# Kernel tuning notes

Measured on AMD Instinct MI355X. Metric: run time of the kernel, lower is better.

The kernel has to match this reference:

```python
import jax, jax.numpy as jnp
import numpy as np

NUM_HEADS = 16
EMB = 1024
HEAD_DIM = EMB // NUM_HEADS


def setup_inputs() -> dict:
    key = jax.random.key(0)
    ks = jax.random.split(key, 9)
    N, L = 2, 2048
    return {
        "keys": jax.random.normal(ks[0], (N, L, EMB), dtype=jnp.float32),
        "queries": jax.random.normal(ks[1], (N, L, EMB), dtype=jnp.float32),
        "values": jax.random.normal(ks[2], (N, L, EMB), dtype=jnp.float32),
        "mask": jax.random.randint(ks[3], (N, L), 0, 2, dtype=jnp.int32),
        "Wk": jax.random.normal(ks[4], (HEAD_DIM, HEAD_DIM), dtype=jnp.float32) * 0.05,
        "Wq": jax.random.normal(ks[5], (HEAD_DIM, HEAD_DIM), dtype=jnp.float32) * 0.05,
        "Wv": jax.random.normal(ks[6], (HEAD_DIM, HEAD_DIM), dtype=jnp.float32) * 0.05,
        "Wo": jax.random.normal(ks[7], (EMB, EMB), dtype=jnp.float32) * 0.02,
        "bo": jax.random.normal(ks[8], (EMB,), dtype=jnp.float32) * 0.02,
    }


def reference(keys, queries, values, mask, Wk, Wq, Wv, Wo, bo):
    N, Q, E = queries.shape
    H, D = NUM_HEADS, HEAD_DIM
    # reshape to heads: [N, L, H, D]
    k = keys.reshape(N, -1, H, D) @ Wk.T
    q = queries.reshape(N, -1, H, D) @ Wq.T
    # faithful to source bug: values are the v-projection of the projected queries
    v = q @ Wv.T
    # energy: [N, H, Q, K]
    energy = jnp.einsum("nqhd,nkhd->nhqk", q, k)
    m = mask[:, None, None, :]  # [N,1,1,K]
    energy = jnp.where(m == 0, jnp.float32(-1e20), energy)
    p = jax.nn.softmax(energy / jnp.sqrt(jnp.float32(E)), axis=3)
    attn = jnp.einsum("nhqk,nkhd->nqhd", p, v).reshape(N, Q, E)
    return attn @ Wo.T + bo
```

## Files before the change

### kernel.cpp

```cpp
#include <hip/hip_runtime.h>
#include <hip/hip_bf16.h>
#include <cmath>

constexpr int N_ = 2;
constexpr int L_ = 2048;
constexpr int H_ = 16;
constexpr int E_ = 1024;
constexpr int ROWS_ = N_ * L_ * H_;
constexpr float KSCALE = 0.04508422002778010648f;

typedef __attribute__((ext_vector_type(8))) short bf16x8;
typedef __attribute__((ext_vector_type(4))) float f32x4;
typedef unsigned short ushort_t;
#define MFMA16(a, b, c) __builtin_amdgcn_mfma_f32_16x16x32_bf16(a, b, c, 0, 0, 0)

__device__ __forceinline__ unsigned short f2bf(float x) {
    union { float f; unsigned u; } v; v.f = x;
    return (unsigned short)((v.u + 0x7fffu + ((v.u >> 16) & 1u)) >> 16);
}
__device__ __forceinline__ unsigned pack2(float a, float b) {
    __hip_bfloat162 t = __float22bfloat162_rn(make_float2(a, b));
    union { __hip_bfloat162 h; unsigned u; } v; v.h = t;
    return v.u;
}
__device__ __forceinline__ void plswap32(unsigned &a, unsigned &b) {
    asm("v_permlane32_swap_b32 %0, %1" : "+v"(a), "+v"(b));
}
__device__ __forceinline__ void plswap16(unsigned &a, unsigned &b) {
    asm("v_permlane16_swap_b32 %0, %1" : "+v"(a), "+v"(b));
}

__global__ __launch_bounds__(256) void proj_kernel(
    const float* __restrict__ keys, const float* __restrict__ queries,
    const float* __restrict__ Wk, const float* __restrict__ Wq, const float* __restrict__ Wv,
    ushort_t* __restrict__ qo, ushort_t* __restrict__ ko, ushort_t* __restrict__ vto)
{
    constexpr int P = 72;
    __shared__ __align__(16) ushort_t Xq[64 * P];
    __shared__ __align__(16) ushort_t Xk[64 * P];
    __shared__ __align__(16) ushort_t Wqs[64 * P];
    __shared__ __align__(16) ushort_t Wks[64 * P];
    __shared__ __align__(16) ushort_t Wvs[64 * P];
    const int tid = threadIdx.x;
    const int lt = blockIdx.x & 31;
    const int h  = (blockIdx.x >> 5) & 15;
    const int n  = blockIdx.x >> 9;
    const int r0 = tid >> 4, c4 = (tid & 15) * 4;

#pragma unroll
    for (int j = 0; j < 4; ++j) {
        const int r = r0 + 16 * j;
        const size_t xoff = (size_t)(n * L_ + lt * 64 + r) * E_ + h * 64 + c4;
        const float4 xq = *(const float4*)&queries[xoff];
        const float4 xk = *(const float4*)&keys[xoff];
        const float4 wq = *(const float4*)&Wq[r * 64 + c4];
        const float4 wk = *(const float4*)&Wk[r * 64 + c4];
        const float4 wv = *(const float4*)&Wv[r * 64 + c4];
        *(uint2*)&Xq[r * P + c4]  = make_uint2(pack2(xq.x, xq.y), pack2(xq.z, xq.w));
        *(uint2*)&Xk[r * P + c4]  = make_uint2(pack2(xk.x, xk.y), pack2(xk.z, xk.w));
        *(uint2*)&Wqs[r * P + c4] = make_uint2(pack2(wq.x, wq.y), pack2(wq.z, wq.w));
        *(uint2*)&Wks[r * P + c4] = make_uint2(pack2(wk.x, wk.y), pack2(wk.z, wk.w));
        *(uint2*)&Wvs[r * P + c4] = make_uint2(pack2(wv.x, wv.y), pack2(wv.z, wv.w));
    }
    __syncthreads();

    const int wave = tid >> 6, lane = tid & 63;
    const int quad = lane >> 4, l16 = lane & 15;
    const int arow = (wave * 16 + l16) * P;
    const f32x4 zero = (f32x4){0.f, 0.f, 0.f, 0.f};

    bf16x8 a0 = *(const bf16x8*)&Xq[arow + quad * 8];
    bf16x8 a1 = *(const bf16x8*)&Xq[arow + 32 + quad * 8];
    bf16x8 c0 = *(const bf16x8*)&Xk[arow + quad * 8];
    bf16x8 c1 = *(const bf16x8*)&Xk[arow + 32 + quad * 8];
    f32x4 qf[4], kf[4];
#pragma unroll
    for (int nt = 0; nt < 4; ++nt) {
        const int brow = (nt * 16 + l16) * P;
        f32x4 acc = MFMA16(a0, *(const bf16x8*)&Wqs[brow + quad * 8], zero);
        qf[nt] = MFMA16(a1, *(const bf16x8*)&Wqs[brow + 32 + quad * 8], acc);
        acc = MFMA16(c0, *(const bf16x8*)&Wks[brow + quad * 8], zero);
        kf[nt] = MFMA16(c1, *(const bf16x8*)&Wks[brow + 32 + quad * 8], acc);
    }
    __syncthreads();

    const int crow = wave * 16 + quad * 4;
#pragma unroll
    for (int nt = 0; nt < 4; ++nt)
#pragma unroll
        for (int reg = 0; reg < 4; ++reg) {
            Xq[(crow + reg) * P + nt * 16 + l16]  = f2bf(qf[nt][reg]);
            Wqs[(crow + reg) * P + nt * 16 + l16] = f2bf(kf[nt][reg] * KSCALE);
        }
    asm volatile("s_waitcnt lgkmcnt(0)" ::: "memory");

    bf16x8 va0 = *(const bf16x8*)&Xq[arow + quad * 8];
    bf16x8 va1 = *(const bf16x8*)&Xq[arow + 32 + quad * 8];
    f32x4 vf[4];
#pragma unroll
    for (int nt = 0; nt < 4; ++nt) {
        const int brow = (nt * 16 + l16) * P;
        f32x4 acc = MFMA16(va0, *(const bf16x8*)&Wvs[brow + quad * 8], zero);
        vf[nt] = MFMA16(va1, *(const bf16x8*)&Wvs[brow + 32 + quad * 8], acc);
    }
#pragma unroll
    for (int nt = 0; nt < 4; ++nt)
#pragma unroll
        for (int reg = 0; reg < 4; ++reg)
            Xk[(nt * 16 + l16) * P + crow + reg] = f2bf(vf[nt][reg]);
    __syncthreads();

#pragma unroll
    for (int j = 0; j < 4; ++j) {
        const int r = r0 + 16 * j;
        const size_t qkoff = (size_t)(n * L_ + lt * 64 + r) * E_ + h * 64 + c4;
        *(uint2*)&qo[qkoff] = *(const uint2*)&Xq[r * P + c4];
        *(uint2*)&ko[qkoff] = *(const uint2*)&Wqs[r * P + c4];
        const size_t vtoff = ((size_t)(n * H_ + h) * 64 + r) * L_ + lt * 64 + c4;
        *(uint2*)&vto[vtoff] = *(const uint2*)&Xk[r * P + c4];
    }
}

__global__ __launch_bounds__(512, 4) void attn_kernel(
    const ushort_t* __restrict__ q, const ushort_t* __restrict__ k,
    const ushort_t* __restrict__ vt, const float* __restrict__ maskf,
    ushort_t* __restrict__ attn)
{
    constexpr int PK = 72;
    constexpr int PV = 136;
    constexpr int KP_SZ = 128 * PK;
    constexpr int VP_SZ = 64 * PV;
    __shared__ __align__(16) unsigned char SMEM[(2 * KP_SZ + 2 * VP_SZ) * 2 + 512];
    ushort_t* Kp = (ushort_t*)SMEM;
    ushort_t* Vp = (ushort_t*)(SMEM + 2 * KP_SZ * 2);
    float*    Ls = (float*)(SMEM + (2 * KP_SZ + 2 * VP_SZ) * 2);
    float*    Oc = (float*)SMEM;
    float*    Lp = (float*)(SMEM + 2 * KP_SZ * 2);

    const int g = blockIdx.x;
    const int xcd = g & 7, j0 = g >> 3;
    const int nh = xcd * 4 + (j0 & 3);
    const int qt = j0 >> 2;
    const int n = nh >> 4, h = nh & 15;

    const int tid = threadIdx.x;
    const int wave = tid >> 6, lane = tid & 63;
    const int l16 = lane & 15, quad = lane >> 4;
    const int qg = wave & 3, kg = wave >> 2;
    const int r8 = tid >> 3, c8 = (tid & 7) * 8;
    const int vr8 = tid >> 4, vc8 = (tid & 15) * 8;

    const ushort_t* kh = k  + (size_t)n * L_ * E_ + h * 64;
    const ushort_t* vh = vt + (size_t)(n * H_ + h) * 64 * L_;
    const float*    mh = maskf + n * L_;
    const size_t qrow0 = (size_t)n * L_ + qt * 128 + qg * 32;

    bf16x8 qb[2][2];
#pragma unroll
    for (int st = 0; st < 2; ++st)
#pragma unroll
        for (int c = 0; c < 2; ++c)
            qb[st][c] = *(const bf16x8*)&q[(qrow0 + st * 16 + l16) * E_ + h * 64 + c * 32 + quad * 8];

    uint4 kr[2], vr[2];
#pragma unroll
    for (int j = 0; j < 2; ++j) {
        kr[j] = *(const uint4*)&kh[(size_t)(64 * j + r8) * E_ + c8];
        vr[j] = *(const uint4*)&vh[(size_t)(vr8 + 32 * j) * L_ + vc8];
    }
    f32x4 mf[4];
#pragma unroll
    for (int mk = 0; mk < 4; ++mk) mf[mk] = *(const f32x4*)&mh[kg * 64 + mk * 16 + quad * 4];

#pragma unroll
    for (int j = 0; j < 2; ++j) {
        *(uint4*)&Kp[(64 * j + r8) * PK + c8]  = kr[j];
        *(uint4*)&Vp[(vr8 + 32 * j) * PV + vc8] = vr[j];
    }
    __syncthreads();

    float lacc[2] = {0.f, 0.f};
    f32x4 O[2][4];
#pragma unroll
    for (int st = 0; st < 2; ++st)
#pragma unroll
        for (int dt = 0; dt < 4; ++dt) O[st][dt] = (f32x4){0.f, 0.f, 0.f, 0.f};

    for (int s = 0; s < 16; ++s) {
        const int cur = s & 1, nxt = cur ^ 1;
        const int sn = (s < 15) ? s + 1 : 15;

#pragma unroll
        for (int j = 0; j < 2; ++j) {
            kr[j] = *(const uint4*)&kh[(size_t)(128 * sn + 64 * j + r8) * E_ + c8];
            vr[j] = *(const uint4*)&vh[(size_t)(vr8 + 32 * j) * L_ + 128 * sn + vc8];
        }
        f32x4 mfn[4];
#pragma unroll
        for (int mk = 0; mk < 4; ++mk)
            mfn[mk] = *(const f32x4*)&mh[128 * sn + kg * 64 + mk * 16 + quad * 4];

        bf16x8 kA[4][2];
#pragma unroll
        for (int mk = 0; mk < 4; ++mk)
#pragma unroll
            for (int c = 0; c < 2; ++c)
                kA[mk][c] = *(const bf16x8*)&Kp[cur * KP_SZ + (kg * 64 + mk * 16 + l16) * PK + c * 32 + quad * 8];

        f32x4 sA[2][4];
#pragma unroll
        for (int st = 0; st < 2; ++st)
#pragma unroll
            for (int mk = 0; mk < 4; ++mk) {
                f32x4 acc = mf[mk];
                acc = MFMA16(kA[mk][0], qb[st][0], acc);
                sA[st][mk] = MFMA16(kA[mk][1], qb[st][1], acc);
            }

        bf16x8 vB[4][2];
#pragma unroll
        for (int dt = 0; dt < 4; ++dt)
#pragma unroll
            for (int c = 0; c < 2; ++c)
                vB[dt][c] = *(const bf16x8*)&Vp[cur * VP_SZ + (dt * 16 + l16) * PV + kg * 64 + c * 32 + quad * 8];

        bf16x8 pa[2][2];
#pragma unroll
        for (int st = 0; st < 2; ++st) {
            unsigned u[4][2];
#pragma unroll
            for (int mk = 0; mk < 4; ++mk) {
                const float p0 = __builtin_amdgcn_exp2f(sA[st][mk][0]);
                const float p1 = __builtin_amdgcn_exp2f(sA[st][mk][1]);
                const float p2 = __builtin_amdgcn_exp2f(sA[st][mk][2]);
                const float p3 = __builtin_amdgcn_exp2f(sA[st][mk][3]);
                lacc[st] += (p0 + p1) + (p2 + p3);
                u[mk][0] = pack2(p0, p1);
                u[mk][1] = pack2(p2, p3);
            }
#pragma unroll
            for (int c = 0; c < 2; ++c) {
                union { unsigned w[4]; bf16x8 v; } pw;
#pragma unroll
                for (int hh = 0; hh < 2; ++hh) {
                    unsigned a = u[2 * c][hh], b = u[2 * c + 1][hh];
                    plswap32(a, b);
                    plswap16(a, b);
                    pw.w[hh] = a; pw.w[2 + hh] = b;
                }
                pa[st][c] = pw.v;
            }
        }

#pragma unroll
        for (int st = 0; st < 2; ++st)
#pragma unroll
            for (int dt = 0; dt < 4; ++dt) {
                O[st][dt] = MFMA16(pa[st][0], vB[dt][0], O[st][dt]);
                O[st][dt] = MFMA16(pa[st][1], vB[dt][1], O[st][dt]);
            }

#pragma unroll
        for (int j = 0; j < 2; ++j) {
            *(uint4*)&Kp[nxt * KP_SZ + (64 * j + r8) * PK + c8]   = kr[j];
            *(uint4*)&Vp[nxt * VP_SZ + (vr8 + 32 * j) * PV + vc8] = vr[j];
        }
#pragma unroll
        for (int mk = 0; mk < 4; ++mk) mf[mk] = mfn[mk];
        __syncthreads();
    }

    float vsum[2];
#pragma unroll
    for (int st = 0; st < 2; ++st) {
        float v = lacc[st];
        v += __shfl_xor(v, 16);
        v += __shfl_xor(v, 32);
        vsum[st] = v;
    }

    if (kg == 1) {
#pragma unroll
        for (int st = 0; st < 2; ++st) {
            if (quad == 0) Lp[qg * 32 + st * 16 + l16] = vsum[st];
#pragma unroll
            for (int dt = 0; dt < 4; ++dt)
                *(f32x4*)&Oc[(dt * 16 + l16) * 132 + qg * 32 + st * 16 + quad * 4] = O[st][dt];
        }
    }
    __syncthreads();

    if (kg == 0) {
#pragma unroll
        for (int st = 0; st < 2; ++st) {
#pragma unroll
            for (int dt = 0; dt < 4; ++dt) {
                const f32x4 op = *(const f32x4*)&Oc[(dt * 16 + l16) * 132 + qg * 32 + st * 16 + quad * 4];
                O[st][dt] += op;
            }
            const float vtot = vsum[st] + Lp[qg * 32 + st * 16 + l16];
            if (quad == 0) Ls[qg * 32 + st * 16 + l16] = 1.f / vtot;
        }
        asm volatile("s_waitcnt lgkmcnt(0)" ::: "memory");
        f32x4 linv[2];
#pragma unroll
        for (int st = 0; st < 2; ++st)
            linv[st] = *(const f32x4*)&Ls[qg * 32 + st * 16 + quad * 4];

#pragma unroll
        for (int st = 0; st < 2; ++st)
#pragma unroll
            for (int dt = 0; dt < 4; ++dt)
#pragma unroll
                for (int reg = 0; reg < 4; ++reg) {
                    const size_t row = qrow0 + st * 16 + quad * 4 + reg;
                    attn[row * E_ + h * 64 + dt * 16 + l16] = f2bf(O[st][dt][reg] * linv[st][reg]);
                }
    }
}

__global__ __launch_bounds__(256) void conv_misc_kernel(
    const float* __restrict__ Wo, const int* __restrict__ mask,
    ushort_t* __restrict__ Wob, float* __restrict__ maskf)
{
    if (blockIdx.x < 1024) {
        const int i = (blockIdx.x * 256 + threadIdx.x) * 4;
        const float4 w = *(const float4*)&Wo[i];
        *(uint2*)&Wob[i] = make_uint2(pack2(w.x, w.y), pack2(w.z, w.w));
    } else {
        const int j = (blockIdx.x - 1024) * 256 + threadIdx.x;
        if (j < N_ * L_) maskf[j] = mask[j] ? 0.f : -1e9f;
    }
}

__global__ __launch_bounds__(256) void outproj_kernel(
    const ushort_t* __restrict__ attn, const ushort_t* __restrict__ Wob,
    const float* __restrict__ bo, float* __restrict__ out)
{
    constexpr int P = 72;
    __shared__ __align__(16) ushort_t As[128 * P];
    __shared__ __align__(16) ushort_t Bs[64 * P];
    const int tid = threadIdx.x;
    const int bc = (blockIdx.x & 15) * 64;
    const int br = (blockIdx.x >> 4) * 128;
    const int r0 = tid >> 4, c4 = (tid & 15) * 4;
    const int wave = tid >> 6, lane = tid & 63;
    const int quad = lane >> 4, l16 = lane & 15;

    uint2 ar[8], brg[4];
#pragma unroll
    for (int j = 0; j < 8; ++j)
        ar[j] = *(const uint2*)&attn[(size_t)(br + r0 + 16 * j) * E_ + c4];
#pragma unroll
    for (int j = 0; j < 4; ++j)
        brg[j] = *(const uint2*)&Wob[(size_t)(bc + r0 + 16 * j) * E_ + c4];

    f32x4 acc[2][4];
#pragma unroll
    for (int s = 0; s < 2; ++s)
#pragma unroll
        for (int nt = 0; nt < 4; ++nt) acc[s][nt] = (f32x4){0.f, 0.f, 0.f, 0.f};

    for (int kt = 0; kt < 16; ++kt) {
#pragma unroll
        for (int j = 0; j < 8; ++j) *(uint2*)&As[(r0 + 16 * j) * P + c4] = ar[j];
#pragma unroll
        for (int j = 0; j < 4; ++j) *(uint2*)&Bs[(r0 + 16 * j) * P + c4] = brg[j];
        __syncthreads();
        const int knext = ((kt < 15) ? (kt + 1) : kt) * 64;
#pragma unroll
        for (int j = 0; j < 8; ++j)
            ar[j] = *(const uint2*)&attn[(size_t)(br + r0 + 16 * j) * E_ + knext + c4];
#pragma unroll
        for (int j = 0; j < 4; ++j)
            brg[j] = *(const uint2*)&Wob[(size_t)(bc + r0 + 16 * j) * E_ + knext + c4];

        bf16x8 aw[2][2], bw[4][2];
#pragma unroll
        for (int s = 0; s < 2; ++s)
#pragma unroll
            for (int c = 0; c < 2; ++c)
                aw[s][c] = *(const bf16x8*)&As[(wave * 32 + s * 16 + l16) * P + c * 32 + quad * 8];
#pragma unroll
        for (int nt = 0; nt < 4; ++nt)
#pragma unroll
            for (int c = 0; c < 2; ++c)
                bw[nt][c] = *(const bf16x8*)&Bs[(nt * 16 + l16) * P + c * 32 + quad * 8];
#pragma unroll
        for (int s = 0; s < 2; ++s)
#pragma unroll
            for (int nt = 0; nt < 4; ++nt) {
                acc[s][nt] = MFMA16(aw[s][0], bw[nt][0], acc[s][nt]);
                acc[s][nt] = MFMA16(aw[s][1], bw[nt][1], acc[s][nt]);
            }
        __syncthreads();
    }
#pragma unroll
    for (int s = 0; s < 2; ++s)
#pragma unroll
        for (int nt = 0; nt < 4; ++nt) {
            const float bias = bo[bc + nt * 16 + l16];
#pragma unroll
            for (int reg = 0; reg < 4; ++reg)
                out[(size_t)(br + wave * 32 + s * 16 + quad * 4 + reg) * E_ + bc + nt * 16 + l16] =
                    acc[s][nt][reg] + bias;
        }
}

extern "C" void kernel_launch(void* const* d_in, const int* in_sizes, int n_in,
                              void* d_out, int out_size, void* d_ws, size_t ws_size,
                              hipStream_t stream)
{
    const float* keys    = (const float*)d_in[0];
    const float* queries = (const float*)d_in[1];
    const int*   mask    = (const int*)d_in[3];
    const float* Wk      = (const float*)d_in[4];
    const float* Wq      = (const float*)d_in[5];
    const float* Wv      = (const float*)d_in[6];
    const float* Wo      = (const float*)d_in[7];
    const float* bo      = (const float*)d_in[8];
    float* out = (float*)d_out;

    ushort_t* qbf  = (ushort_t*)d_ws;
    ushort_t* kbf  = qbf + (size_t)ROWS_ * 64;
    ushort_t* vtbf = kbf + (size_t)ROWS_ * 64;
    ushort_t* abf  = vtbf + (size_t)ROWS_ * 64;
    ushort_t* wob  = abf + (size_t)ROWS_ * 64;
    float*    mskf = (float*)(wob + (size_t)E_ * E_);

    conv_misc_kernel<<<1024 + (N_ * L_ + 255) / 256, 256, 0, stream>>>(Wo, mask, wob, mskf);
    proj_kernel<<<N_ * H_ * (L_ / 64), 256, 0, stream>>>(keys, queries, Wk, Wq, Wv,
                                                         qbf, kbf, vtbf);
    attn_kernel<<<N_ * H_ * (L_ / 128), 512, 0, stream>>>(qbf, kbf, vtbf, mskf, abf);
    outproj_kernel<<<(N_ * L_ / 128) * (E_ / 64), 256, 0, stream>>>(abf, wob, bo, out);
}
```

Before: 183.4 us.

## Fuse conversion kernel into projection, compute row sums via MFMA, widen loads

Folds the Wo bf16 conversion and mask preprocessing into the projection kernel as extra blocks, removing one kernel launch. In attention, the softmax denominator is now accumulated with an MFMA against a ones vector instead of scalar adds plus cross-lane shuffles, and s_setprio hints are placed around the MFMA sections. The output projection switches from 8-byte to 16-byte global and LDS accesses, and its MFMA loop is also wrapped with setprio. In exchange the attention loop issues extra MFMAs and the projection kernel runs a larger, mixed-work grid.

```diff
diff --git a/kernel.cpp b/kernel.cpp
--- a/kernel.cpp
+++ b/kernel.cpp
@@ -33,7 +33,9 @@
 __global__ __launch_bounds__(256) void proj_kernel(
     const float* __restrict__ keys, const float* __restrict__ queries,
     const float* __restrict__ Wk, const float* __restrict__ Wq, const float* __restrict__ Wv,
-    ushort_t* __restrict__ qo, ushort_t* __restrict__ ko, ushort_t* __restrict__ vto)
+    ushort_t* __restrict__ qo, ushort_t* __restrict__ ko, ushort_t* __restrict__ vto,
+    const float* __restrict__ Wo, const int* __restrict__ mask,
+    ushort_t* __restrict__ Wob, float* __restrict__ maskf)
 {
     constexpr int P = 72;
     __shared__ __align__(16) ushort_t Xq[64 * P];
@@ -42,6 +44,20 @@
     __shared__ __align__(16) ushort_t Wks[64 * P];
     __shared__ __align__(16) ushort_t Wvs[64 * P];
     const int tid = threadIdx.x;
+
+    if (blockIdx.x >= 1024) {
+        const int b = blockIdx.x - 1024;
+        if (b < 1024) {
+            const int i = (b * 256 + tid) * 4;
+            const float4 w = *(const float4*)&Wo[i];
+            *(uint2*)&Wob[i] = make_uint2(pack2(w.x, w.y), pack2(w.z, w.w));
+        } else {
+            const int j = (b - 1024) * 256 + tid;
+            if (j < N_ * L_) maskf[j] = mask[j] ? 0.f : -1e9f;
+        }
+        return;
+    }
+
     const int lt = blockIdx.x & 31;
     const int h  = (blockIdx.x >> 5) & 15;
     const int n  = blockIdx.x >> 9;
@@ -130,10 +146,9 @@
     constexpr int PV = 136;
     constexpr int KP_SZ = 128 * PK;
     constexpr int VP_SZ = 64 * PV;
-    __shared__ __align__(16) unsigned char SMEM[(2 * KP_SZ + 2 * VP_SZ) * 2 + 512];
+    __shared__ __align__(16) unsigned char SMEM[(2 * KP_SZ + 2 * VP_SZ) * 2];
     ushort_t* Kp = (ushort_t*)SMEM;
     ushort_t* Vp = (ushort_t*)(SMEM + 2 * KP_SZ * 2);
-    float*    Ls = (float*)(SMEM + (2 * KP_SZ + 2 * VP_SZ) * 2);
     float*    Oc = (float*)SMEM;
     float*    Lp = (float*)(SMEM + 2 * KP_SZ * 2);
 
@@ -155,6 +170,10 @@
     const float*    mh = maskf + n * L_;
     const size_t qrow0 = (size_t)n * L_ + qt * 128 + qg * 32;
 
+    bf16x8 onesB;
+#pragma unroll
+    for (int i = 0; i < 8; ++i) onesB[i] = (short)0x3F80;
+
     bf16x8 qb[2][2];
 #pragma unroll
     for (int st = 0; st < 2; ++st)
@@ -179,12 +198,13 @@
     }
     __syncthreads();
 
-    float lacc[2] = {0.f, 0.f};
-    f32x4 O[2][4];
-#pragma unroll
-    for (int st = 0; st < 2; ++st)
+    f32x4 O[2][4], lO[2];
+#pragma unroll
+    for (int st = 0; st < 2; ++st) {
+        lO[st] = (f32x4){0.f, 0.f, 0.f, 0.f};
 #pragma unroll
         for (int dt = 0; dt < 4; ++dt) O[st][dt] = (f32x4){0.f, 0.f, 0.f, 0.f};
+    }
 
     for (int s = 0; s < 16; ++s) {
         const int cur = s & 1, nxt = cur ^ 1;
@@ -208,6 +228,7 @@
                 kA[mk][c] = *(const bf16x8*)&Kp[cur * KP_SZ + (kg * 64 + mk * 16 + l16) * PK + c * 32 + quad * 8];
 
         f32x4 sA[2][4];
+        __builtin_amdgcn_s_setprio(1);
 #pragma unroll
         for (int st = 0; st < 2; ++st)
 #pragma unroll
@@ -216,6 +237,7 @@
                 acc = MFMA16(kA[mk][0], qb[st][0], acc);
                 sA[st][mk] = MFMA16(kA[mk][1], qb[st][1], acc);
             }
+        __builtin_amdgcn_s_setprio(0);
 
         bf16x8 vB[4][2];
 #pragma unroll
@@ -234,7 +256,6 @@
                 const float p1 = __builtin_amdgcn_exp2f(sA[st][mk][1]);
                 const float p2 = __builtin_amdgcn_exp2f(sA[st][mk][2]);
                 const float p3 = __builtin_amdgcn_exp2f(sA[st][mk][3]);
-                lacc[st] += (p0 + p1) + (p2 + p3);
                 u[mk][0] = pack2(p0, p1);
                 u[mk][1] = pack2(p2, p3);
             }
@@ -252,13 +273,18 @@
             }
         }
 
-#pragma unroll
-        for (int st = 0; st < 2; ++st)
+        __builtin_amdgcn_s_setprio(1);
+#pragma unroll
+        for (int st = 0; st < 2; ++st) {
 #pragma unroll
             for (int dt = 0; dt < 4; ++dt) {
                 O[st][dt] = MFMA16(pa[st][0], vB[dt][0], O[st][dt]);
                 O[st][dt] = MFMA16(pa[st][1], vB[dt][1], O[st][dt]);
             }
+            lO[st] = MFMA16(pa[st][0], onesB, lO[st]);
+            lO[st] = MFMA16(pa[st][1], onesB, lO[st]);
+        }
+        __builtin_amdgcn_s_setprio(0);
 
 #pragma unroll
         for (int j = 0; j < 2; ++j) {
@@ -270,27 +296,20 @@
         __syncthreads();
     }
 
-    float vsum[2];
-#pragma unroll
-    for (int st = 0; st < 2; ++st) {
-        float v = lacc[st];
-        v += __shfl_xor(v, 16);
-        v += __shfl_xor(v, 32);
-        vsum[st] = v;
-    }
-
     if (kg == 1) {
 #pragma unroll
         for (int st = 0; st < 2; ++st) {
-            if (quad == 0) Lp[qg * 32 + st * 16 + l16] = vsum[st];
 #pragma unroll
             for (int dt = 0; dt < 4; ++dt)
                 *(f32x4*)&Oc[(dt * 16 + l16) * 132 + qg * 32 + st * 16 + quad * 4] = O[st][dt];
+            if (l16 == 0)
+                *(f32x4*)&Lp[qg * 32 + st * 16 + quad * 4] = lO[st];
         }
     }
     __syncthreads();
 
     if (kg == 0) {
+        f32x4 linv[2];
 #pragma unroll
         for (int st = 0; st < 2; ++st) {
 #pragma unroll
@@ -298,14 +317,11 @@
                 const f32x4 op = *(const f32x4*)&Oc[(dt * 16 + l16) * 132 + qg * 32 + st * 16 + quad * 4];
                 O[st][dt] += op;
             }
-            const float vtot = vsum[st] + Lp[qg * 32 + st * 16 + l16];
-            if (quad == 0) Ls[qg * 32 + st * 16 + l16] = 1.f / vtot;
-        }
-        asm volatile("s_waitcnt lgkmcnt(0)" ::: "memory");
-        f32x4 linv[2];
-#pragma unroll
-        for (int st = 0; st < 2; ++st)
-            linv[st] = *(const f32x4*)&Ls[qg * 32 + st * 16 + quad * 4];
+            const f32x4 lpart = *(const f32x4*)&Lp[qg * 32 + st * 16 + quad * 4];
+#pragma unroll
+            for (int reg = 0; reg < 4; ++reg)
+                linv[st][reg] = 1.f / (lO[st][reg] + lpart[reg]);
+        }
 
 #pragma unroll
         for (int st = 0; st < 2; ++st)
@@ -316,20 +332,6 @@
                     const size_t row = qrow0 + st * 16 + quad * 4 + reg;
                     attn[row * E_ + h * 64 + dt * 16 + l16] = f2bf(O[st][dt][reg] * linv[st][reg]);
                 }
-    }
-}
-
-__global__ __launch_bounds__(256) void conv_misc_kernel(
-    const float* __restrict__ Wo, const int* __restrict__ mask,
-    ushort_t* __restrict__ Wob, float* __restrict__ maskf)
-{
-    if (blockIdx.x < 1024) {
-        const int i = (blockIdx.x * 256 + threadIdx.x) * 4;
-        const float4 w = *(const float4*)&Wo[i];
-        *(uint2*)&Wob[i] = make_uint2(pack2(w.x, w.y), pack2(w.z, w.w));
-    } else {
-        const int j = (blockIdx.x - 1024) * 256 + threadIdx.x;
-        if (j < N_ * L_) maskf[j] = mask[j] ? 0.f : -1e9f;
     }
 }
 
@@ -343,17 +345,17 @@
     const int tid = threadIdx.x;
     const int bc = (blockIdx.x & 15) * 64;
     const int br = (blockIdx.x >> 4) * 128;
-    const int r0 = tid >> 4, c4 = (tid & 15) * 4;
+    const int rt = tid >> 3, ct = (tid & 7) * 8;
     const int wave = tid >> 6, lane = tid & 63;
     const int quad = lane >> 4, l16 = lane & 15;
 
-    uint2 ar[8], brg[4];
-#pragma unroll
-    for (int j = 0; j < 8; ++j)
-        ar[j] = *(const uint2*)&attn[(size_t)(br + r0 + 16 * j) * E_ + c4];
+    uint4 ar[4], brg[2];
 #pragma unroll
     for (int j = 0; j < 4; ++j)
-        brg[j] = *(const uint2*)&Wob[(size_t)(bc + r0 + 16 * j) * E_ + c4];
+        ar[j] = *(const uint4*)&attn[(size_t)(br + rt + 32 * j) * E_ + ct];
+#pragma unroll
+    for (int j = 0; j < 2; ++j)
+        brg[j] = *(const uint4*)&Wob[(size_t)(bc + rt + 32 * j) * E_ + ct];
 
     f32x4 acc[2][4];
 #pragma unroll
@@ -363,17 +365,17 @@
 
     for (int kt = 0; kt < 16; ++kt) {
 #pragma unroll
-        for (int j = 0; j < 8; ++j) *(uint2*)&As[(r0 + 16 * j) * P + c4] = ar[j];
-#pragma unroll
-        for (int j = 0; j < 4; ++j) *(uint2*)&Bs[(r0 + 16 * j) * P + c4] = brg[j];
+        for (int j = 0; j < 4; ++j) *(uint4*)&As[(rt + 32 * j) * P + ct] = ar[j];
+#pragma unroll
+        for (int j = 0; j < 2; ++j) *(uint4*)&Bs[(rt + 32 * j) * P + ct] = brg[j];
         __syncthreads();
         const int knext = ((kt < 15) ? (kt + 1) : kt) * 64;
 #pragma unroll
-        for (int j = 0; j < 8; ++j)
-            ar[j] = *(const uint2*)&attn[(size_t)(br + r0 + 16 * j) * E_ + knext + c4];
-#pragma unroll
         for (int j = 0; j < 4; ++j)
-            brg[j] = *(const uint2*)&Wob[(size_t)(bc + r0 + 16 * j) * E_ + knext + c4];
+            ar[j] = *(const uint4*)&attn[(size_t)(br + rt + 32 * j) * E_ + knext + ct];
+#pragma unroll
+        for (int j = 0; j < 2; ++j)
+            brg[j] = *(const uint4*)&Wob[(size_t)(bc + rt + 32 * j) * E_ + knext + ct];
 
         bf16x8 aw[2][2], bw[4][2];
 #pragma unroll
@@ -386,6 +388,7 @@
 #pragma unroll
             for (int c = 0; c < 2; ++c)
                 bw[nt][c] = *(const bf16x8*)&Bs[(nt * 16 + l16) * P + c * 32 + quad * 8];
+        __builtin_amdgcn_s_setprio(1);
 #pragma unroll
         for (int s = 0; s < 2; ++s)
 #pragma unroll
@@ -393,6 +396,7 @@
                 acc[s][nt] = MFMA16(aw[s][0], bw[nt][0], acc[s][nt]);
                 acc[s][nt] = MFMA16(aw[s][1], bw[nt][1], acc[s][nt]);
             }
+        __builtin_amdgcn_s_setprio(0);
         __syncthreads();
     }
 #pragma unroll
@@ -428,9 +432,8 @@
     ushort_t* wob  = abf + (size_t)ROWS_ * 64;
     float*    mskf = (float*)(wob + (size_t)E_ * E_);
 
-    conv_misc_kernel<<<1024 + (N_ * L_ + 255) / 256, 256, 0, stream>>>(Wo, mask, wob, mskf);
-    proj_kernel<<<N_ * H_ * (L_ / 64), 256, 0, stream>>>(keys, queries, Wk, Wq, Wv,
-                                                         qbf, kbf, vtbf);
+    proj_kernel<<<1024 + 1024 + (N_ * L_ + 255) / 256, 256, 0, stream>>>(
+        keys, queries, Wk, Wq, Wv, qbf, kbf, vtbf, Wo, mask, wob, mskf);
     attn_kernel<<<N_ * H_ * (L_ / 128), 512, 0, stream>>>(qbf, kbf, vtbf, mskf, abf);
     outproj_kernel<<<(N_ * L_ / 128) * (E_ / 64), 256, 0, stream>>>(abf, wob, bo, out);
 }
```

Measured after the change: 433.0 us. +136.0%, slower.
